# Kernel optimization log

Hardware: AMD Instinct MI355X
Metric: run time of the kernel (lower is better)

The kernel has to match this reference:

```python
import jax, jax.numpy as jnp
import numpy as np

B, N, E, D, R = 32, 2048, 8192, 512, 8
V_SENSE = 25000
V_GLOBAL = 50000  # last_idx_globals - last_idx_senses


def setup_inputs() -> dict:
    key = jax.random.key(0)
    ks = jax.random.split(key, 12)
    x = jax.random.normal(ks[0], (B, N, D), dtype=jnp.float32)
    edge_index = jax.random.randint(ks[1], (B, 2, E), 0, N)
    edge_type = jax.random.randint(ks[2], (B, E), 0, R)
    s = 0.02
    basis = jax.random.normal(ks[3], (R, D, D), dtype=jnp.float32) * s   # num_bases = R
    comp = jax.random.normal(ks[4], (R, R), dtype=jnp.float32) * s      # [num_relations, num_bases]
    root = jax.random.normal(ks[5], (D, D), dtype=jnp.float32) * s
    bias_conv = jnp.zeros((D,), dtype=jnp.float32)
    w_global = jax.random.normal(ks[6], (V_GLOBAL, D), dtype=jnp.float32) * s
    b_global = jnp.zeros((V_GLOBAL,), dtype=jnp.float32)
    w_sense = jax.random.normal(ks[7], (V_SENSE, D), dtype=jnp.float32) * s
    b_sense = jnp.zeros((V_SENSE,), dtype=jnp.float32)
    return {"x": x, "edge_index": edge_index, "edge_type": edge_type,
            "basis": basis, "comp": comp, "root": root, "bias_conv": bias_conv,
            "w_global": w_global, "b_global": b_global,
            "w_sense": w_sense, "b_sense": b_sense}


def reference(x, edge_index, edge_type, basis, comp, root, bias_conv,
              w_global, b_global, w_sense, b_sense):
    # Basis decomposition: per-relation weight W_r = sum_b comp[r,b] * basis[b]
    W = jnp.einsum('rb,bio->rio', comp, basis)  # [R, D, D]

    def conv_one(xg, ei, et):
        # RGCNConv with mean aggregation per relation + root transform + bias
        src, dst = ei[0], ei[1]
        x_src = xg[src]                              # [E, D] gather
        out = xg @ root + bias_conv                  # [N, D]
        for r in range(R):                           # fixed small relation loop
            mask = (et == r).astype(xg.dtype)        # [E]
            msg = (x_src @ W[r]) * mask[:, None]     # [E, D]
            s = jax.ops.segment_sum(msg, dst, num_segments=N)              # [N, D]
            cnt = jax.ops.segment_sum(mask, dst, num_segments=N)           # [N]
            out = out + s / jnp.maximum(cnt, 1.0)[:, None]                 # mean aggr
        return out

    h = jax.vmap(conv_one)(x, edge_index, edge_type)  # [B, N, D]
    h = jax.nn.relu(h)
    h0 = h[:, 0]                                      # current node per sample [B, D]
    logits_global = h0 @ w_global.T + b_global        # [B, V_GLOBAL]
    logits_sense = h0 @ w_sense.T + b_sense           # [B, V_SENSE]
    return (jax.nn.log_softmax(logits_global, axis=-1),
            jax.nn.log_softmax(logits_sense, axis=-1))
```

## Files before the change

kernel.cpp:

```cpp
#include <hip/hip_runtime.h>
#include <hip/hip_bf16.h>

#define BATCH 32
#define NNODE 2048
#define NEDGE 8192
#define DIM   512
#define NREL  8
#define VG    50000
#define VS    25000
#define ZI    4608
#define NCH   36
#define GB5   782
#define SB5   391
#define PG    25
#define PS    13

typedef __attribute__((ext_vector_type(4))) float f32x4;
typedef __attribute__((ext_vector_type(8))) short s16x8;

__global__ __launch_bounds__(512) void k_conv(const float* __restrict__ x,
                                              const int* __restrict__ ei,
                                              const int* __restrict__ et,
                                              const float* __restrict__ comp,
                                              float* __restrict__ z) {
    int g = blockIdx.x;
    int t = threadIdx.x;
    int wv = t >> 6, lane = t & 63;
    __shared__ int elds[8 * 128];
    __shared__ int wcnt[8];
    const int* srcp = ei + (size_t)(g * 2 + 0) * NEDGE;
    const int* dstp = ei + (size_t)(g * 2 + 1) * NEDGE;

    int run = 0;
    for (int it = 0; it < 16; it++) {
        int e = wv * 1024 + it * 64 + lane;
        bool m = (dstp[e] == 0);
        unsigned long long mask = __ballot(m);
        int rank = __popcll(mask & ((1ull << lane) - 1ull));
        if (m && (run + rank) < 128) elds[wv * 128 + run + rank] = e;
        run += (int)__popcll(mask);
    }
    if (lane == 0) wcnt[wv] = (run > 128) ? 128 : run;
    __syncthreads();

    int d = t;
    float s0=0,s1=0,s2=0,s3=0,s4=0,s5=0,s6=0,s7=0;
    int   c0=0,c1=0,c2=0,c3=0,c4=0,c5=0,c6=0,c7=0;
    for (int w = 0; w < 8; w++) {
        int cw = wcnt[w];
        for (int i = 0; i < cw; i++) {
            int e = elds[w * 128 + i];
            int r = et[(size_t)g * NEDGE + e];
            int sn = srcp[e];
            float val = x[((size_t)g * NNODE + sn) * DIM + d];
            if (r == 0) { s0 += val; c0++; }
            if (r == 1) { s1 += val; c1++; }
            if (r == 2) { s2 += val; c2++; }
            if (r == 3) { s3 += val; c3++; }
            if (r == 4) { s4 += val; c4++; }
            if (r == 5) { s5 += val; c5++; }
            if (r == 6) { s6 += val; c6++; }
            if (r == 7) { s7 += val; c7++; }
        }
    }
    float sv[8] = {s0,s1,s2,s3,s4,s5,s6,s7};
    float inv[8];
    int   cv[8] = {c0,c1,c2,c3,c4,c5,c6,c7};
    #pragma unroll
    for (int r = 0; r < 8; r++) inv[r] = 1.0f / fmaxf((float)cv[r], 1.0f);

    z[(size_t)g * ZI + d] = x[((size_t)g * NNODE + 0) * DIM + d];
    #pragma unroll
    for (int b = 0; b < 8; b++) {
        float y = 0.f;
        #pragma unroll
        for (int r = 0; r < 8; r++) y += comp[r * 8 + b] * inv[r] * sv[r];
        z[(size_t)g * ZI + 512 + b * 512 + d] = y;
    }
}

__global__ __launch_bounds__(512) void k_gemm_part(const float* __restrict__ z,
                                                   const float* __restrict__ root,
                                                   const float* __restrict__ basis,
                                                   float* __restrict__ part2) {
    int bx = blockIdx.x;
    int dt = bx & 3;
    int cc = bx >> 2;
    int t = threadIdx.x;
    int dl = t & 127, gq = t >> 7;
    __shared__ float ztT[128][33];
    #pragma unroll
    for (int rep = 0; rep < 8; rep++) {
        int flat = rep * 512 + t;
        int g = flat >> 7, i = flat & 127;
        ztT[i][g] = z[(size_t)g * ZI + cc * 128 + i];
    }
    __syncthreads();
    const float* M = (cc < 4) ? (root + (size_t)(cc * 128) * 512)
                              : (basis + (size_t)((cc - 4) * 128) * 512);
    float acc[8] = {0,0,0,0,0,0,0,0};
    for (int i = 0; i < 128; i++) {
        float m = M[(size_t)i * 512 + dt * 128 + dl];
        #pragma unroll
        for (int j = 0; j < 8; j++) acc[j] += ztT[i][gq * 8 + j] * m;
    }
    #pragma unroll
    for (int j = 0; j < 8; j++) {
        int g = gq * 8 + j;
        part2[((size_t)cc * 32 + g) * 512 + dt * 128 + dl] = acc[j];
    }
}

__device__ __forceinline__ unsigned bf16rne(float f) {
    unsigned u = __float_as_uint(f);
    return (u + 0x7FFFu + ((u >> 16) & 1u)) >> 16;
}

__global__ __launch_bounds__(256) void k_h0(const float* __restrict__ part2,
                                            const float* __restrict__ bias_conv,
                                            unsigned* __restrict__ h0t) {
    int g = blockIdx.x;
    int p = threadIdx.x;
    int d0 = 2 * p;
    float v0 = bias_conv[d0], v1 = bias_conv[d0 + 1];
    for (int cc = 0; cc < NCH; cc++) {
        const float* pp = part2 + ((size_t)cc * 32 + g) * 512 + d0;
        v0 += pp[0];
        v1 += pp[1];
    }
    v0 = fmaxf(v0, 0.f);
    v1 = fmaxf(v1, 0.f);
    h0t[g * 256 + p] = bf16rne(v0) | (bf16rne(v1) << 16);
}

__device__ __forceinline__ short f2bf(float f) {
    __hip_bfloat16 h = __float2bfloat16(f);
    return *reinterpret_cast<short*>(&h);
}

__global__ __launch_bounds__(256, 4) void k_logits5(const unsigned* __restrict__ h0t,
                                                    const float* __restrict__ wg,
                                                    const float* __restrict__ bg,
                                                    const float* __restrict__ wsn,
                                                    const float* __restrict__ bsv,
                                                    float* __restrict__ out) {
    __shared__ __align__(16) unsigned char hlds[32768];

    int t = threadIdx.x;
    int bx = blockIdx.x;
    int wv = t >> 6, l = t & 63;

    const float* w; const float* bias; float* ob; int V; int v0;
    if (bx < GB5) { w = wg;  bias = bg;  ob = out;                      V = VG; v0 = bx * 64; }
    else          { w = wsn; bias = bsv; ob = out + (size_t)BATCH * VG; V = VS; v0 = (bx - GB5) * 64; }

    #pragma unroll
    for (int rep = 0; rep < 8; rep++) {
        int idx = rep * 256 + t;
        int g = idx >> 6, q = idx & 63;
        uint4 val = *(const uint4*)&h0t[idx * 4];
        *(uint4*)&hlds[g * 1024 + ((q ^ (g & 7)) << 4)] = val;
    }
    __syncthreads();

    int c  = l & 15;
    int kg = l >> 4;
    int vb = v0 + wv * 16 + c;
    int vr = (vb < V) ? vb : (V - 1);
    const float4* __restrict__ wrow = (const float4*)(w + (size_t)vr * 512);
    int swz = c & 7;
    const unsigned char* ha = &hlds[c * 1024];
    const unsigned char* hb = &hlds[(c + 16) * 1024];

    f32x4 acc0 = {0.f, 0.f, 0.f, 0.f};
    f32x4 acc1 = {0.f, 0.f, 0.f, 0.f};

    #pragma unroll
    for (int kc = 0; kc < 16; kc++) {
        float4 b0 = wrow[kc * 8 + kg * 2];
        float4 b1 = wrow[kc * 8 + kg * 2 + 1];
        int gr = ((kc * 4 + kg) ^ swz) << 4;
        s16x8 a0 = *(const s16x8*)(ha + gr);
        s16x8 a1 = *(const s16x8*)(hb + gr);
        s16x8 bf;
        bf[0] = f2bf(b0.x); bf[1] = f2bf(b0.y); bf[2] = f2bf(b0.z); bf[3] = f2bf(b0.w);
        bf[4] = f2bf(b1.x); bf[5] = f2bf(b1.y); bf[6] = f2bf(b1.z); bf[7] = f2bf(b1.w);
        acc0 = __builtin_amdgcn_mfma_f32_16x16x32_bf16(a0, bf, acc0, 0, 0, 0);
        acc1 = __builtin_amdgcn_mfma_f32_16x16x32_bf16(a1, bf, acc1, 0, 0, 0);
    }

    if (vb < V) {
        float bia = bias[vb];
        #pragma unroll
        for (int j = 0; j < 4; j++) {
            int g0 = kg * 4 + j;
            ob[(size_t)g0 * V + vb]        = acc0[j] + bia;
            ob[(size_t)(g0 + 16) * V + vb] = acc1[j] + bia;
        }
    }
}

__global__ __launch_bounds__(256) void k_lse_part(const float* __restrict__ out,
                                                  float* __restrict__ part) {
    int bx = blockIdx.x;
    int V, ci, pidx;
    const float* row;
    if (bx < 32 * PG) {
        int g = bx / PG; ci = bx % PG; V = VG;
        row = out + (size_t)g * VG;
        pidx = g * PG + ci;
    } else {
        int b2 = bx - 32 * PG;
        int g = b2 / PS; ci = b2 % PS; V = VS;
        row = out + (size_t)BATCH * VG + (size_t)g * VS;
        pidx = 32 * PG + g * PS + ci;
    }
    int t = threadIdx.x;
    float p = 0.f;
    int base = ci * 2048 + t * 8;
    #pragma unroll
    for (int jj = 0; jj < 8; jj++) {
        int idx = base + jj;
        if (idx < V) p += expf(row[idx]);
    }
    #pragma unroll
    for (int s = 1; s < 64; s <<= 1) p += __shfl_xor(p, s);
    __shared__ float wsum[4];
    if ((t & 63) == 0) wsum[t >> 6] = p;
    __syncthreads();
    if (t == 0) part[pidx] = wsum[0] + wsum[1] + wsum[2] + wsum[3];
}

__global__ __launch_bounds__(64) void k_lse_final(const float* __restrict__ part,
                                                  float* __restrict__ lse) {
    int t = threadIdx.x;
    int head = t >> 5, g = t & 31;
    float s = 0.f;
    if (head == 0) { for (int c = 0; c < PG; c++) s += part[g * PG + c]; }
    else           { for (int c = 0; c < PS; c++) s += part[32 * PG + g * PS + c]; }
    lse[t] = logf(s);
}

__global__ __launch_bounds__(256) void k_sub(float* __restrict__ out,
                                             const float* __restrict__ lse) {
    unsigned i4 = blockIdx.x * 256u + threadIdx.x;
    if (i4 >= 600000u) return;
    unsigned idx = i4 * 4u;
    float l;
    if (idx < 1600000u) l = lse[idx / 50000u];
    else                l = lse[32u + (idx - 1600000u) / 25000u];
    float4 v = *(float4*)(out + idx);
    v.x -= l; v.y -= l; v.z -= l; v.w -= l;
    *(float4*)(out + idx) = v;
}

extern "C" void kernel_launch(void* const* d_in, const int* in_sizes, int n_in,
                              void* d_out, int out_size, void* d_ws, size_t ws_size,
                              hipStream_t stream) {
    const float* x        = (const float*)d_in[0];
    const int*   ei       = (const int*)  d_in[1];
    const int*   et       = (const int*)  d_in[2];
    const float* basis    = (const float*)d_in[3];
    const float* comp     = (const float*)d_in[4];
    const float* root     = (const float*)d_in[5];
    const float* biasc    = (const float*)d_in[6];
    const float* wg       = (const float*)d_in[7];
    const float* bg       = (const float*)d_in[8];
    const float* wsn      = (const float*)d_in[9];
    const float* bsv      = (const float*)d_in[10];
    float* out = (float*)d_out;

    float* z     = out;
    float* part2 = out + (size_t)BATCH * ZI;
    unsigned* h0t  = (unsigned*)d_ws;
    float*    plse = (float*)d_ws + 8192;
    float*    lse  = plse + 32 * PG + 32 * PS;

    k_conv     <<<BATCH, 512, 0, stream>>>(x, ei, et, comp, z);
    k_gemm_part<<<NCH * 4, 512, 0, stream>>>(z, root, basis, part2);
    k_h0       <<<BATCH, 256, 0, stream>>>(part2, biasc, h0t);
    k_logits5  <<<GB5 + SB5, 256, 0, stream>>>(h0t, wg, bg, wsn, bsv, out);
    k_lse_part <<<32 * PG + 32 * PS, 256, 0, stream>>>(out, plse);
    k_lse_final<<<1, 64, 0, stream>>>(plse, lse);
    k_sub      <<<2344, 256, 0, stream>>>(out, lse);
}
```

Measured before the change: 77.79 us.

## Stage logits weights via direct global-to-LDS loads and split-K across waves

The logits kernel now covers 16 vocab rows per block instead of 64, loading each block's weight rows straight into shared memory with global_load_lds. The four waves split the K dimension and combine partial MFMA results through an LDS reduction before adding bias and writing out. This aims at better memory-level parallelism and coalescing on the weight stream, which is the dominant traffic. In exchange it launches four times as many blocks, uses much more LDS per block (lower occupancy, launch bound cut to 2), restages h0 in every block, and adds a reduction and barrier.

```diff
diff --git a/kernel.cpp b/kernel.cpp
--- a/kernel.cpp
+++ b/kernel.cpp
@@ -10,10 +10,11 @@
 #define VS    25000
 #define ZI    4608
 #define NCH   36
-#define GB5   782
-#define SB5   391
+#define GB6   3125
+#define SB6   1563
 #define PG    25
 #define PS    13
+#define WROWB 2064
 
 typedef __attribute__((ext_vector_type(4))) float f32x4;
 typedef __attribute__((ext_vector_type(8))) short s16x8;
@@ -133,26 +134,46 @@
     h0t[g * 256 + p] = bf16rne(v0) | (bf16rne(v1) << 16);
 }
 
+__device__ __forceinline__ void gload_lds16(const float* gsrc, float* ldst) {
+    __builtin_amdgcn_global_load_lds(
+        (const __attribute__((address_space(1))) void*)gsrc,
+        (__attribute__((address_space(3))) void*)ldst,
+        16, 0, 0);
+}
+
 __device__ __forceinline__ short f2bf(float f) {
     __hip_bfloat16 h = __float2bfloat16(f);
     return *reinterpret_cast<short*>(&h);
 }
 
-__global__ __launch_bounds__(256, 4) void k_logits5(const unsigned* __restrict__ h0t,
+__global__ __launch_bounds__(256, 2) void k_logits6(const unsigned* __restrict__ h0t,
                                                     const float* __restrict__ wg,
                                                     const float* __restrict__ bg,
                                                     const float* __restrict__ wsn,
                                                     const float* __restrict__ bsv,
                                                     float* __restrict__ out) {
     __shared__ __align__(16) unsigned char hlds[32768];
+    __shared__ __align__(16) unsigned char wlds[16 * WROWB];
+    __shared__ __align__(16) float redbuf[2048];
 
     int t = threadIdx.x;
     int bx = blockIdx.x;
     int wv = t >> 6, l = t & 63;
 
     const float* w; const float* bias; float* ob; int V; int v0;
-    if (bx < GB5) { w = wg;  bias = bg;  ob = out;                      V = VG; v0 = bx * 64; }
-    else          { w = wsn; bias = bsv; ob = out + (size_t)BATCH * VG; V = VS; v0 = (bx - GB5) * 64; }
+    if (bx < GB6) { w = wg;  bias = bg;  ob = out;                      V = VG; v0 = bx * 16; }
+    else          { w = wsn; bias = bsv; ob = out + (size_t)BATCH * VG; V = VS; v0 = (bx - GB6) * 16; }
+    int Vm1 = V - 1;
+
+    #pragma unroll
+    for (int j = 0; j < 8; j++) {
+        int i   = wv * 8 + j;
+        int row = i >> 1;
+        int kh  = i & 1;
+        int vr  = v0 + row; if (vr > Vm1) vr = Vm1;
+        const float* src = w + (size_t)vr * 512 + kh * 256 + l * 4;
+        gload_lds16(src, (float*)&wlds[row * WROWB + kh * 1024]);
+    }
 
     #pragma unroll
     for (int rep = 0; rep < 8; rep++) {
@@ -165,9 +186,6 @@
 
     int c  = l & 15;
     int kg = l >> 4;
-    int vb = v0 + wv * 16 + c;
-    int vr = (vb < V) ? vb : (V - 1);
-    const float4* __restrict__ wrow = (const float4*)(w + (size_t)vr * 512);
     int swz = c & 7;
     const unsigned char* ha = &hlds[c * 1024];
     const unsigned char* hb = &hlds[(c + 16) * 1024];
@@ -176,12 +194,14 @@
     f32x4 acc1 = {0.f, 0.f, 0.f, 0.f};
 
     #pragma unroll
-    for (int kc = 0; kc < 16; kc++) {
-        float4 b0 = wrow[kc * 8 + kg * 2];
-        float4 b1 = wrow[kc * 8 + kg * 2 + 1];
+    for (int j = 0; j < 4; j++) {
+        int kc = wv * 4 + j;
         int gr = ((kc * 4 + kg) ^ swz) << 4;
         s16x8 a0 = *(const s16x8*)(ha + gr);
         s16x8 a1 = *(const s16x8*)(hb + gr);
+        const float4* bp = (const float4*)&wlds[c * WROWB + kc * 128 + kg * 32];
+        float4 b0 = bp[0];
+        float4 b1 = bp[1];
         s16x8 bf;
         bf[0] = f2bf(b0.x); bf[1] = f2bf(b0.y); bf[2] = f2bf(b0.z); bf[3] = f2bf(b0.w);
         bf[4] = f2bf(b1.x); bf[5] = f2bf(b1.y); bf[6] = f2bf(b1.z); bf[7] = f2bf(b1.w);
@@ -189,13 +209,31 @@
         acc1 = __builtin_amdgcn_mfma_f32_16x16x32_bf16(a1, bf, acc1, 0, 0, 0);
     }
 
-    if (vb < V) {
-        float bia = bias[vb];
+    {
+        float* rb = redbuf + wv * 512;
+        int ro = c * 16 + kg * 4;
+        *(f32x4*)&rb[ro]       = acc0;
+        *(f32x4*)&rb[256 + ro] = acc1;
+    }
+    __syncthreads();
+
+    {
+        int grp = t >> 7;
+        int cc  = (t & 127) >> 3;
+        int r2  = (t & 7) * 2;
+        float s0 = 0.f, s1 = 0.f;
         #pragma unroll
-        for (int j = 0; j < 4; j++) {
-            int g0 = kg * 4 + j;
-            ob[(size_t)g0 * V + vb]        = acc0[j] + bia;
-            ob[(size_t)(g0 + 16) * V + vb] = acc1[j] + bia;
+        for (int kw = 0; kw < 4; kw++) {
+            int base = kw * 512 + grp * 256 + cc * 16 + r2;
+            s0 += redbuf[base];
+            s1 += redbuf[base + 1];
+        }
+        int vv = v0 + cc;
+        if (vv < V) {
+            float bia = bias[vv];
+            int g = grp * 16 + r2;
+            ob[(size_t)g * V + vv]       = s0 + bia;
+            ob[(size_t)(g + 1) * V + vv] = s1 + bia;
         }
     }
 }
@@ -279,7 +317,7 @@
     k_conv     <<<BATCH, 512, 0, stream>>>(x, ei, et, comp, z);
     k_gemm_part<<<NCH * 4, 512, 0, stream>>>(z, root, basis, part2);
     k_h0       <<<BATCH, 256, 0, stream>>>(part2, biasc, h0t);
-    k_logits5  <<<GB5 + SB5, 256, 0, stream>>>(h0t, wg, bg, wsn, bsv, out);
+    k_logits6  <<<GB6 + SB6, 256, 0, stream>>>(h0t, wg, bg, wsn, bsv, out);
     k_lse_part <<<32 * PG + 32 * PS, 256, 0, stream>>>(out, plse);
     k_lse_final<<<1, 64, 0, stream>>>(plse, lse);
     k_sub      <<<2344, 256, 0, stream>>>(out, lse);
```

Result: no change. 77.96 us (+0.2%).

## Fuse exp-sum partials into logits GEMM and prefetch weights with nontemporal loads

Applied to the files above, without the earlier changes.

The logits kernel now computes per-tile exp sums in its epilogue and writes 32-row partials, which replaces the separate pass that re-read the full logits array to build exp sums. Weight rows are software-prefetched four k-chunks ahead with nontemporal loads to hide latency on the streaming weight reads. Tiles are assigned per wave, so global and sense tiles can mix within a block and the ragged tail is handled at 16-column granularity. The final LSE reduction becomes 64 blocks reading a larger partial buffer. The fused sum uses __expf without max subtraction, the same unstabilised form as before.

```diff
diff --git a/kernel.cpp b/kernel.cpp
--- a/kernel.cpp
+++ b/kernel.cpp
@@ -10,10 +10,10 @@
 #define VS    25000
 #define ZI    4608
 #define NCH   36
-#define GB5   782
-#define SB5   391
-#define PG    25
-#define PS    13
+#define NT_G  3125
+#define NT_S  1563
+#define TTOT  4688
+#define NBLK8 1172
 
 typedef __attribute__((ext_vector_type(4))) float f32x4;
 typedef __attribute__((ext_vector_type(8))) short s16x8;
@@ -138,21 +138,17 @@
     return *reinterpret_cast<short*>(&h);
 }
 
-__global__ __launch_bounds__(256, 4) void k_logits5(const unsigned* __restrict__ h0t,
+__global__ __launch_bounds__(256, 4) void k_logits8(const unsigned* __restrict__ h0t,
                                                     const float* __restrict__ wg,
                                                     const float* __restrict__ bg,
                                                     const float* __restrict__ wsn,
                                                     const float* __restrict__ bsv,
-                                                    float* __restrict__ out) {
+                                                    float* __restrict__ out,
+                                                    float* __restrict__ part) {
     __shared__ __align__(16) unsigned char hlds[32768];
 
     int t = threadIdx.x;
-    int bx = blockIdx.x;
     int wv = t >> 6, l = t & 63;
-
-    const float* w; const float* bias; float* ob; int V; int v0;
-    if (bx < GB5) { w = wg;  bias = bg;  ob = out;                      V = VG; v0 = bx * 64; }
-    else          { w = wsn; bias = bsv; ob = out + (size_t)BATCH * VG; V = VS; v0 = (bx - GB5) * 64; }
 
     #pragma unroll
     for (int rep = 0; rep < 8; rep++) {
@@ -163,82 +159,97 @@
     }
     __syncthreads();
 
+    int tile = blockIdx.x * 4 + wv;
+    const float* w; const float* bias; float* ob; int V; int v0;
+    if (tile < NT_G) { w = wg;  bias = bg;  ob = out;                      V = VG; v0 = tile * 16; }
+    else             { w = wsn; bias = bsv; ob = out + (size_t)BATCH * VG; V = VS; v0 = (tile - NT_G) * 16; }
+
     int c  = l & 15;
     int kg = l >> 4;
-    int vb = v0 + wv * 16 + c;
+    int vb = v0 + c;
     int vr = (vb < V) ? vb : (V - 1);
-    const float4* __restrict__ wrow = (const float4*)(w + (size_t)vr * 512);
+    const f32x4* __restrict__ wrow = (const f32x4*)(w + (size_t)vr * 512) + kg * 2;
     int swz = c & 7;
     const unsigned char* ha = &hlds[c * 1024];
     const unsigned char* hb = &hlds[(c + 16) * 1024];
 
+    f32x4 wb[4][2];
+    #pragma unroll
+    for (int p = 0; p < 4; p++) {
+        wb[p][0] = __builtin_nontemporal_load(&wrow[p * 8]);
+        wb[p][1] = __builtin_nontemporal_load(&wrow[p * 8 + 1]);
+    }
+
     f32x4 acc0 = {0.f, 0.f, 0.f, 0.f};
     f32x4 acc1 = {0.f, 0.f, 0.f, 0.f};
 
     #pragma unroll
     for (int kc = 0; kc < 16; kc++) {
-        float4 b0 = wrow[kc * 8 + kg * 2];
-        float4 b1 = wrow[kc * 8 + kg * 2 + 1];
+        f32x4 b0 = wb[kc & 3][0];
+        f32x4 b1 = wb[kc & 3][1];
+        if (kc + 4 < 16) {
+            wb[kc & 3][0] = __builtin_nontemporal_load(&wrow[(kc + 4) * 8]);
+            wb[kc & 3][1] = __builtin_nontemporal_load(&wrow[(kc + 4) * 8 + 1]);
+        }
         int gr = ((kc * 4 + kg) ^ swz) << 4;
         s16x8 a0 = *(const s16x8*)(ha + gr);
         s16x8 a1 = *(const s16x8*)(hb + gr);
         s16x8 bf;
-        bf[0] = f2bf(b0.x); bf[1] = f2bf(b0.y); bf[2] = f2bf(b0.z); bf[3] = f2bf(b0.w);
-        bf[4] = f2bf(b1.x); bf[5] = f2bf(b1.y); bf[6] = f2bf(b1.z); bf[7] = f2bf(b1.w);
+        bf[0] = f2bf(b0[0]); bf[1] = f2bf(b0[1]); bf[2] = f2bf(b0[2]); bf[3] = f2bf(b0[3]);
+        bf[4] = f2bf(b1[0]); bf[5] = f2bf(b1[1]); bf[6] = f2bf(b1[2]); bf[7] = f2bf(b1[3]);
         acc0 = __builtin_amdgcn_mfma_f32_16x16x32_bf16(a0, bf, acc0, 0, 0, 0);
         acc1 = __builtin_amdgcn_mfma_f32_16x16x32_bf16(a1, bf, acc1, 0, 0, 0);
     }
 
-    if (vb < V) {
-        float bia = bias[vb];
+    float p0[4], p1[4];
+    bool valid = (vb < V);
+    float bia = valid ? bias[vb] : 0.f;
+    #pragma unroll
+    for (int j = 0; j < 4; j++) {
+        float v0f = acc0[j] + bia;
+        float v1f = acc1[j] + bia;
+        int g0 = kg * 4 + j;
+        if (valid) {
+            ob[(size_t)g0 * V + vb]        = v0f;
+            ob[(size_t)(g0 + 16) * V + vb] = v1f;
+        }
+        p0[j] = valid ? __expf(v0f) : 0.f;
+        p1[j] = valid ? __expf(v1f) : 0.f;
+    }
+    #pragma unroll
+    for (int s = 1; s < 16; s <<= 1) {
         #pragma unroll
         for (int j = 0; j < 4; j++) {
-            int g0 = kg * 4 + j;
-            ob[(size_t)g0 * V + vb]        = acc0[j] + bia;
-            ob[(size_t)(g0 + 16) * V + vb] = acc1[j] + bia;
-        }
-    }
-}
-
-__global__ __launch_bounds__(256) void k_lse_part(const float* __restrict__ out,
-                                                  float* __restrict__ part) {
+            p0[j] += __shfl_xor(p0[j], s);
+            p1[j] += __shfl_xor(p1[j], s);
+        }
+    }
+    if (c == 0) {
+        float* pt = part + (size_t)tile * 32;
+        #pragma unroll
+        for (int j = 0; j < 4; j++) {
+            pt[kg * 4 + j]      = p0[j];
+            pt[kg * 4 + j + 16] = p1[j];
+        }
+    }
+}
+
+__global__ __launch_bounds__(256) void k_lse64(const float* __restrict__ part,
+                                               float* __restrict__ lse) {
     int bx = blockIdx.x;
-    int V, ci, pidx;
-    const float* row;
-    if (bx < 32 * PG) {
-        int g = bx / PG; ci = bx % PG; V = VG;
-        row = out + (size_t)g * VG;
-        pidx = g * PG + ci;
-    } else {
-        int b2 = bx - 32 * PG;
-        int g = b2 / PS; ci = b2 % PS; V = VS;
-        row = out + (size_t)BATCH * VG + (size_t)g * VS;
-        pidx = 32 * PG + g * PS + ci;
-    }
-    int t = threadIdx.x;
-    float p = 0.f;
-    int base = ci * 2048 + t * 8;
-    #pragma unroll
-    for (int jj = 0; jj < 8; jj++) {
-        int idx = base + jj;
-        if (idx < V) p += expf(row[idx]);
-    }
-    #pragma unroll
-    for (int s = 1; s < 64; s <<= 1) p += __shfl_xor(p, s);
-    __shared__ float wsum[4];
-    if ((t & 63) == 0) wsum[t >> 6] = p;
-    __syncthreads();
-    if (t == 0) part[pidx] = wsum[0] + wsum[1] + wsum[2] + wsum[3];
-}
-
-__global__ __launch_bounds__(64) void k_lse_final(const float* __restrict__ part,
-                                                  float* __restrict__ lse) {
-    int t = threadIdx.x;
-    int head = t >> 5, g = t & 31;
+    int head = bx >> 5, g = bx & 31;
+    int tbase = head ? NT_G : 0;
+    int ntl   = head ? (TTOT - NT_G) : NT_G;
+    int t = threadIdx.x;
     float s = 0.f;
-    if (head == 0) { for (int c = 0; c < PG; c++) s += part[g * PG + c]; }
-    else           { for (int c = 0; c < PS; c++) s += part[32 * PG + g * PS + c]; }
-    lse[t] = logf(s);
+    for (int i = t; i < ntl; i += 256)
+        s += part[(size_t)(tbase + i) * 32 + g];
+    #pragma unroll
+    for (int m = 1; m < 64; m <<= 1) s += __shfl_xor(s, m);
+    __shared__ float ws4[4];
+    if ((t & 63) == 0) ws4[t >> 6] = s;
+    __syncthreads();
+    if (t == 0) lse[bx] = logf(ws4[0] + ws4[1] + ws4[2] + ws4[3]);
 }
 
 __global__ __launch_bounds__(256) void k_sub(float* __restrict__ out,
@@ -273,14 +284,13 @@
     float* z     = out;
     float* part2 = out + (size_t)BATCH * ZI;
     unsigned* h0t  = (unsigned*)d_ws;
-    float*    plse = (float*)d_ws + 8192;
-    float*    lse  = plse + 32 * PG + 32 * PS;
+    float*    part = (float*)d_ws + 8192;
+    float*    lse  = part + (size_t)TTOT * 32;
 
     k_conv     <<<BATCH, 512, 0, stream>>>(x, ei, et, comp, z);
     k_gemm_part<<<NCH * 4, 512, 0, stream>>>(z, root, basis, part2);
     k_h0       <<<BATCH, 256, 0, stream>>>(part2, biasc, h0t);
-    k_logits5  <<<GB5 + SB5, 256, 0, stream>>>(h0t, wg, bg, wsn, bsv, out);
-    k_lse_part <<<32 * PG + 32 * PS, 256, 0, stream>>>(out, plse);
-    k_lse_final<<<1, 64, 0, stream>>>(plse, lse);
+    k_logits8  <<<NBLK8, 256, 0, stream>>>(h0t, wg, bg, wsn, bsv, out, part);
+    k_lse64    <<<64, 256, 0, stream>>>(part, lse);
     k_sub      <<<2344, 256, 0, stream>>>(out, lse);
 }
```

New measurement: 78.24 us. No clear change (+0.6%).
